# Kernel optimization log

Hardware: AMD Instinct MI355X
Metric: run time of the kernel (lower is better)

The kernel has to match this reference:

```python
import jax, jax.numpy as jnp
import numpy as np

DIM = 768
HEAD = 12
DK = DIM // HEAD

def setup_inputs() -> dict:
    key = jax.random.key(0)
    ks = jax.random.split(key, 9)
    B, L = 4, 2048
    s = 1.0 / np.sqrt(DIM)
    qkv = jax.random.normal(ks[0], (B, L, DIM), dtype=jnp.float32)
    mask = jnp.ones((B, L), dtype=jnp.int32)
    Wq = jax.random.normal(ks[1], (DIM, DIM), dtype=jnp.float32) * s
    bq = jnp.zeros((DIM,), dtype=jnp.float32)
    Wk = jax.random.normal(ks[2], (DIM, DIM), dtype=jnp.float32) * s
    bk = jnp.zeros((DIM,), dtype=jnp.float32)
    Wv = jax.random.normal(ks[3], (DIM, DIM), dtype=jnp.float32) * s
    bv = jnp.zeros((DIM,), dtype=jnp.float32)
    Wo = jax.random.normal(ks[4], (DIM, DIM), dtype=jnp.float32) * s
    bo = jnp.zeros((DIM,), dtype=jnp.float32)
    return {"qkv": qkv, "mask": mask, "Wq": Wq, "bq": bq, "Wk": Wk, "bk": bk,
            "Wv": Wv, "bv": bv, "Wo": Wo, "bo": bo}

def reference(qkv, mask, Wq, bq, Wk, bk, Wv, bv, Wo, bo):
    B, L, _ = qkv.shape
    def proj(W, b):
        # [B,L,dim] -> [B,H,L,dk]
        return (qkv @ W + b).reshape(B, L, HEAD, DK).transpose(0, 2, 1, 3)
    q, k, v = proj(Wq, bq), proj(Wk, bk), proj(Wv, bv)
    scores = jnp.einsum('bhqd,bhkd->bhqk', q, k) / jnp.sqrt(jnp.float32(DK))
    # mask: [B,L] broadcast over heads and query positions (key axis)
    m = mask[:, None, None, :]  # [B,1,1,L]
    scores = jnp.where(m == 0, jnp.float32(-1e9), scores)
    p = jax.nn.softmax(scores, axis=-1)
    x = jnp.einsum('bhqk,bhkd->bhqd', p, v)  # [B,H,L,dk]
    x = x.transpose(0, 2, 1, 3).reshape(B, L, DIM)
    return x @ Wo + bo
```

## Files before the change

### kernel.cpp

```cpp
#include <hip/hip_runtime.h>
#include <hip/hip_bf16.h>
#include <stdint.h>

#define DIM  768
#define NHEAD 12
#define DK   64
#define BATCH 4
#define SEQ  2048
#define ROWS (BATCH*SEQ)
#define SCL  0.1803368801111204f

typedef __bf16 bf16_t;
typedef bf16_t bf16x8 __attribute__((ext_vector_type(8)));
typedef bf16_t bf16x4 __attribute__((ext_vector_type(4)));
typedef float  f32x4  __attribute__((ext_vector_type(4)));
typedef float  f32x16 __attribute__((ext_vector_type(16)));

typedef unsigned int __attribute__((address_space(1)))* as1p;
typedef unsigned int __attribute__((address_space(3)))* as3p;

__device__ __forceinline__ void gload_lds16(const void* g, void* l) {
    __builtin_amdgcn_global_load_lds((as1p)g, (as3p)l, 16, 0, 0);
}
#define MEMFENCE asm volatile("" ::: "memory")

__global__ void cast_bf16_kernel(const float* __restrict__ in, bf16_t* __restrict__ out) {
    int i = blockIdx.x * 256 + threadIdx.x;
    const float4* p = (const float4*)in;
    float4 a = p[(size_t)i*2], b = p[(size_t)i*2+1];
    bf16x8 v;
    v[0]=(bf16_t)a.x; v[1]=(bf16_t)a.y; v[2]=(bf16_t)a.z; v[3]=(bf16_t)a.w;
    v[4]=(bf16_t)b.x; v[5]=(bf16_t)b.y; v[6]=(bf16_t)b.z; v[7]=(bf16_t)b.w;
    *(bf16x8*)(out + (size_t)i*8) = v;
}

__global__ void wtrans_kernel(const float* __restrict__ W0, const float* __restrict__ W1,
                              const float* __restrict__ W2, const float* __restrict__ W3,
                              bf16_t* __restrict__ T0, bf16_t* __restrict__ T1,
                              bf16_t* __restrict__ T2, bf16_t* __restrict__ T3) {
    const float* W = blockIdx.z==0?W0 : blockIdx.z==1?W1 : blockIdx.z==2?W2 : W3;
    bf16_t*      T = blockIdx.z==0?T0 : blockIdx.z==1?T1 : blockIdx.z==2?T2 : T3;
    __shared__ float tile[32][33];
    int tx = threadIdx.x, ty = threadIdx.y;
    int c = blockIdx.x*32 + tx;
    #pragma unroll
    for (int r = 0; r < 32; r += 8)
        tile[ty+r][tx] = W[(size_t)(blockIdx.y*32 + ty + r)*DIM + c];
    __syncthreads();
    int oc = blockIdx.y*32 + tx;
    #pragma unroll
    for (int r = 0; r < 32; r += 8)
        T[(size_t)(blockIdx.x*32 + ty + r)*DIM + oc] = (bf16_t)tile[tx][ty+r];
}

template<int MODE>
__global__ __launch_bounds__(256) void gemm_kernel(
    const bf16_t* __restrict__ A,
    const bf16_t* __restrict__ WTa, const bf16_t* __restrict__ WTb, const bf16_t* __restrict__ WTc,
    const float* __restrict__ ba, const float* __restrict__ bb, const float* __restrict__ bc,
    bf16_t* __restrict__ Qo, bf16_t* __restrict__ Ko, bf16_t* __restrict__ Vo,
    float* __restrict__ Oo) {
    __shared__ __align__(16) bf16_t As[128*64];
    __shared__ __align__(16) bf16_t Bs[128*64];
    const int tid = threadIdx.x, wave = tid>>6, lane = tid&63;
    const int wm = wave>>1, wn = wave&1;
    const int m0 = blockIdx.x*128, n0 = blockIdx.y*128;
    const int z = (MODE==0) ? (int)blockIdx.z : 0;
    const bf16_t* WT  = (z==0) ? WTa : (z==1 ? WTb : WTc);
    const float* bias = (z==0) ? ba  : (z==1 ? bb  : bc);

    f32x4 acc[4][4];
    const f32x4 zf = {0.f,0.f,0.f,0.f};
    #pragma unroll
    for (int m = 0; m < 4; ++m)
        #pragma unroll
        for (int n = 0; n < 4; ++n) acc[m][n] = zf;

    const int srow = wave*32 + (lane>>3);
    const int scol = (lane&7)*8;
    const bf16_t* Ag = A  + (size_t)(m0+srow)*DIM + scol;
    const bf16_t* Bg = WT + (size_t)(n0+srow)*DIM + scol;
    bf16_t* AsW = As + (wave*32)*64;
    bf16_t* BsW = Bs + (wave*32)*64;

    for (int k0 = 0; k0 < DIM; k0 += 64) {
        __syncthreads();
        #pragma unroll
        for (int i = 0; i < 4; ++i) {
            gload_lds16(Ag + (size_t)(i*8)*DIM + k0, AsW + i*8*64);
            gload_lds16(Bg + (size_t)(i*8)*DIM + k0, BsW + i*8*64);
        }
        __syncthreads();
        #pragma unroll
        for (int ks = 0; ks < 2; ++ks) {
            bf16x8 af[4], bfr[4];
            #pragma unroll
            for (int m = 0; m < 4; ++m)
                af[m]  = *(const bf16x8*)&As[(wm*64 + m*16 + (lane&15))*64 + ks*32 + (lane>>4)*8];
            #pragma unroll
            for (int n = 0; n < 4; ++n)
                bfr[n] = *(const bf16x8*)&Bs[(wn*64 + n*16 + (lane&15))*64 + ks*32 + (lane>>4)*8];
            #pragma unroll
            for (int m = 0; m < 4; ++m)
                #pragma unroll
                for (int n = 0; n < 4; ++n)
                    acc[m][n] = __builtin_amdgcn_mfma_f32_16x16x32_bf16(af[m], bfr[n], acc[m][n], 0, 0, 0);
        }
    }

    float bvv[4];
    #pragma unroll
    for (int n = 0; n < 4; ++n) bvv[n] = bias[n0 + wn*64 + n*16 + (lane&15)];

    #pragma unroll
    for (int m = 0; m < 4; ++m) {
        #pragma unroll
        for (int n = 0; n < 4; ++n) {
            #pragma unroll
            for (int r = 0; r < 4; ++r) {
                float val = acc[m][n][r] + bvv[n];
                int R = m0 + wm*64 + m*16 + (lane>>4)*4 + r;
                int C = n0 + wn*64 + n*16 + (lane&15);
                if (MODE == 1) {
                    Oo[(size_t)R*DIM + C] = val;
                } else {
                    int bi = R>>11, li = R&2047, h = C>>6, d = C&63;
                    size_t bh = (size_t)(bi*NHEAD + h);
                    if      (z==0) Qo[(bh*SEQ + li)*DK + d] = (bf16_t)(val*SCL);
                    else if (z==1) Ko[(bh*SEQ + li)*DK + d] = (bf16_t)val;
                    else {
                        int li2 = (li & ~12) | ((li&4)<<1) | ((li&8)>>1);
                        Vo[(bh*DK + d)*SEQ + li2] = (bf16_t)val;
                    }
                }
            }
        }
    }
}

#define NT (SEQ/64)

__global__ __launch_bounds__(256) void attn_kernel(
    const bf16_t* __restrict__ Q, const bf16_t* __restrict__ K, const bf16_t* __restrict__ VT,
    const int* __restrict__ mask, bf16_t* __restrict__ X) {
    __shared__ __align__(16) bf16_t lds[2*8192];
    const int tid = threadIdx.x, wv = tid>>6, lane = tid&63;
    const int lo5 = lane&31, hi5 = lane>>5;
    const int bh = blockIdx.y, bi = bh/NHEAD, h = bh%NHEAD;
    const bf16_t* Qb = Q  + (size_t)bh*SEQ*DK;
    const bf16_t* Kb = K  + (size_t)bh*SEQ*DK;
    const bf16_t* Vb = VT + (size_t)bh*DK*SEQ;
    const int* mk = mask + (size_t)bi*SEQ + lo5;
    const int q0 = blockIdx.x*128 + wv*32;

    bf16x8 qf[4];
    #pragma unroll
    for (int ks = 0; ks < 4; ++ks)
        qf[ks] = *(const bf16x8*)&Qb[(size_t)(q0 + lo5)*DK + ks*16 + hi5*8];

    f32x16 O0, O1;
    #pragma unroll
    for (int r = 0; r < 16; ++r) { O0[r] = 0.f; O1[r] = 0.f; }
    float mrun = -1e30f, lsum = 0.f;

    bf16x8 onesb = {};
    if (hi5 == 0) onesb[0] = (bf16_t)1.0f;

    const int srow  = wv*16 + (lane>>3);
    const int sslot = (lane&7) ^ (srow&7);
    const bf16_t* Kg = Kb + (size_t)srow*DK  + sslot*8;
    const bf16_t* Vg = Vb + (size_t)srow*SEQ + sslot*8;
    int koff[4];
    #pragma unroll
    for (int ks = 0; ks < 4; ++ks) koff[ks] = (((2*ks + hi5) ^ (lo5 & 7)) << 3);

    #pragma unroll
    for (int i = 0; i < 2; ++i) {
        gload_lds16(Kg + (size_t)(i*8)*DK,  lds +        (wv*16 + i*8)*64);
        gload_lds16(Vg + (size_t)(i*8)*SEQ, lds + 4096 + (wv*16 + i*8)*64);
    }

    int cur = 0;
    for (int t = 0; t < NT; ++t) {
        const int kv0 = t*64;
        int mv0 = mk[kv0], mv1 = mk[kv0 + 32];
        if (t < NT-1) {
            bf16_t* nb = lds + (cur^1)*8192;
            #pragma unroll
            for (int i = 0; i < 2; ++i) {
                gload_lds16(Kg + (size_t)(kv0+64)*DK + (size_t)(i*8)*DK,  nb +        (wv*16 + i*8)*64);
                gload_lds16(Vg + (kv0+64)            + (size_t)(i*8)*SEQ, nb + 4096 + (wv*16 + i*8)*64);
            }
            asm volatile("s_waitcnt vmcnt(4)" ::: "memory");
        } else {
            asm volatile("s_waitcnt vmcnt(0)" ::: "memory");
        }
        MEMFENCE; __builtin_amdgcn_s_barrier(); MEMFENCE;

        const bf16_t* Kt = lds + cur*8192;
        const bf16_t* Vt = lds + cur*8192 + 4096;

        f32x16 s0, s1;
        #pragma unroll
        for (int r = 0; r < 16; ++r) { s0[r] = 0.f; s1[r] = 0.f; }
        #pragma unroll
        for (int ks = 0; ks < 4; ++ks) {
            bf16x8 a0 = *(const bf16x8*)&Kt[ lo5     *64 + koff[ks]];
            bf16x8 a1 = *(const bf16x8*)&Kt[(32+lo5)*64 + koff[ks]];
            s0 = __builtin_amdgcn_mfma_f32_32x32x16_bf16(a0, qf[ks], s0, 0, 0, 0);
            s1 = __builtin_amdgcn_mfma_f32_32x32x16_bf16(a1, qf[ks], s1, 0, 0, 0);
        }
        bf16x8 ba = {};
        ba[0] = mv0 ? (bf16_t)0.f : (bf16_t)(-1024.0f);
        s0 = __builtin_amdgcn_mfma_f32_32x32x16_bf16(ba, onesb, s0, 0, 0, 0);
        ba[0] = mv1 ? (bf16_t)0.f : (bf16_t)(-1024.0f);
        s1 = __builtin_amdgcn_mfma_f32_32x32x16_bf16(ba, onesb, s1, 0, 0, 0);

        float pm = fmaxf(s0[0], s1[0]);
        #pragma unroll
        for (int r = 1; r < 16; ++r) pm = fmaxf(pm, fmaxf(s0[r], s1[r]));
        pm = fmaxf(pm, __shfl_xor(pm, 32));

        float nm = fmaxf(mrun, pm);
        if (__any(pm > mrun + 8.f)) {
            float fs = __builtin_amdgcn_exp2f(mrun - nm);
            lsum *= fs;
            #pragma unroll
            for (int r = 0; r < 16; ++r) { O0[r] *= fs; O1[r] *= fs; }
            mrun = nm;
        }
        float ps = 0.f;
        #pragma unroll
        for (int r = 0; r < 16; ++r) {
            s0[r] = __builtin_amdgcn_exp2f(s0[r] - mrun);
            s1[r] = __builtin_amdgcn_exp2f(s1[r] - mrun);
            ps += s0[r] + s1[r];
        }
        lsum += ps + __shfl_xor(ps, 32);

        bf16x8 pf0, pf1, pf2, pf3;
        #pragma unroll
        for (int j = 0; j < 8; ++j) {
            pf0[j] = (bf16_t)s0[j];
            pf1[j] = (bf16_t)s0[8+j];
            pf2[j] = (bf16_t)s1[j];
            pf3[j] = (bf16_t)s1[8+j];
        }

        #pragma unroll
        for (int ks = 0; ks < 4; ++ks) {
            bf16x8 pb = (ks==0) ? pf0 : (ks==1) ? pf1 : (ks==2) ? pf2 : pf3;
            bf16x8 a0 = *(const bf16x8*)&Vt[ lo5     *64 + koff[ks]];
            bf16x8 a1 = *(const bf16x8*)&Vt[(32+lo5)*64 + koff[ks]];
            O0 = __builtin_amdgcn_mfma_f32_32x32x16_bf16(a0, pb, O0, 0, 0, 0);
            O1 = __builtin_amdgcn_mfma_f32_32x32x16_bf16(a1, pb, O1, 0, 0, 0);
        }
        MEMFENCE; __builtin_amdgcn_s_barrier(); MEMFENCE;
        cur ^= 1;
    }

    float rl = __builtin_amdgcn_rcpf(lsum);
    const size_t rowb = (size_t)(bi*SEQ + q0 + lo5)*DIM + h*DK;
    #pragma unroll
    for (int g = 0; g < 4; ++g) {
        bf16x4 v0, v1;
        #pragma unroll
        for (int j = 0; j < 4; ++j) {
            v0[j] = (bf16_t)(O0[g*4+j] * rl);
            v1[j] = (bf16_t)(O1[g*4+j] * rl);
        }
        *(bf16x4*)&X[rowb + g*8 + hi5*4]      = v0;
        *(bf16x4*)&X[rowb + 32 + g*8 + hi5*4] = v1;
    }
}

extern "C" void kernel_launch(void* const* d_in, const int* in_sizes, int n_in,
                              void* d_out, int out_size, void* d_ws, size_t ws_size,
                              hipStream_t stream) {
    (void)in_sizes; (void)n_in; (void)out_size; (void)ws_size;
    const float* qkv = (const float*)d_in[0];
    const int*  mask = (const int*)d_in[1];
    const float* Wq = (const float*)d_in[2];
    const float* bq = (const float*)d_in[3];
    const float* Wk = (const float*)d_in[4];
    const float* bk = (const float*)d_in[5];
    const float* Wv = (const float*)d_in[6];
    const float* bv = (const float*)d_in[7];
    const float* Wo = (const float*)d_in[8];
    const float* bo = (const float*)d_in[9];
    float* out = (float*)d_out;

    char* ws = (char*)d_ws;
    size_t off = 0;
    auto carve = [&](size_t bytes) { void* p = ws + off; off += (bytes + 255) & ~(size_t)255; return p; };
    const size_t actN = (size_t)ROWS*DIM;
    bf16_t* Abf = (bf16_t*)carve(actN*2);
    bf16_t* WTq = (bf16_t*)carve((size_t)DIM*DIM*2);
    bf16_t* WTk = (bf16_t*)carve((size_t)DIM*DIM*2);
    bf16_t* WTv = (bf16_t*)carve((size_t)DIM*DIM*2);
    bf16_t* WTo = (bf16_t*)carve((size_t)DIM*DIM*2);
    bf16_t* Qb  = (bf16_t*)carve(actN*2);
    bf16_t* Kb  = (bf16_t*)carve(actN*2);
    bf16_t* VTb = (bf16_t*)carve(actN*2);
    bf16_t* Xb  = (bf16_t*)carve(actN*2);

    cast_bf16_kernel<<<dim3(ROWS*DIM/8/256), dim3(256), 0, stream>>>(qkv, Abf);
    wtrans_kernel<<<dim3(24,24,4), dim3(32,8), 0, stream>>>(Wq, Wk, Wv, Wo, WTq, WTk, WTv, WTo);
    gemm_kernel<0><<<dim3(64,6,3), dim3(256), 0, stream>>>(Abf, WTq, WTk, WTv, bq, bk, bv,
                                                           Qb, Kb, VTb, nullptr);
    attn_kernel<<<dim3(16,48), dim3(256), 0, stream>>>(Qb, Kb, VTb, mask, Xb);
    gemm_kernel<1><<<dim3(64,6,1), dim3(256), 0, stream>>>(Xb, WTo, WTo, WTo, bo, bo, bo,
                                                           nullptr, nullptr, nullptr, out);
}
```

Measured before the change: 199.1 us.

## Skip mask bias MFMAs when batch mask is all ones, remap blocks per XCD

Each attention block first scans its batch's mask row and, if every entry is nonzero, skips the per-tile mask loads and the two extra bias MFMAs. The 2D grid is flattened to 1D and remapped so that blocks sharing one head land on the same XCD, which should improve K/V reuse in L2. The max and sum reductions are rewritten as trees to shorten dependency chains. The mask scan adds a small prologue read per block. The skip stays correct for any mask because it falls back when zeros are present.

```diff
diff --git a/kernel.cpp b/kernel.cpp
--- a/kernel.cpp
+++ b/kernel.cpp
@@ -146,12 +146,26 @@
     __shared__ __align__(16) bf16_t lds[2*8192];
     const int tid = threadIdx.x, wv = tid>>6, lane = tid&63;
     const int lo5 = lane&31, hi5 = lane>>5;
-    const int bh = blockIdx.y, bi = bh/NHEAD, h = bh%NHEAD;
+    const int b = blockIdx.x;
+    const int xcd = b & 7, ii = b >> 3;
+    const int bh = xcd*6 + (ii>>4), qt = ii & 15;
+    const int bi = bh/NHEAD, h = bh%NHEAD;
     const bf16_t* Qb = Q  + (size_t)bh*SEQ*DK;
     const bf16_t* Kb = K  + (size_t)bh*SEQ*DK;
     const bf16_t* Vb = VT + (size_t)bh*DK*SEQ;
     const int* mk = mask + (size_t)bi*SEQ + lo5;
-    const int q0 = blockIdx.x*128 + wv*32;
+    const int q0 = qt*128 + wv*32;
+
+    int mOk = 1;
+    {
+        const int4* m4 = (const int4*)(mask + (size_t)bi*SEQ);
+        #pragma unroll
+        for (int i2 = 0; i2 < 8; ++i2) {
+            int4 v = m4[lane + i2*64];
+            mOk &= (v.x != 0) & (v.y != 0) & (v.z != 0) & (v.w != 0);
+        }
+    }
+    const int mAll = __all(mOk);
 
     bf16x8 qf[4];
     #pragma unroll
@@ -183,7 +197,6 @@
     int cur = 0;
     for (int t = 0; t < NT; ++t) {
         const int kv0 = t*64;
-        int mv0 = mk[kv0], mv1 = mk[kv0 + 32];
         if (t < NT-1) {
             bf16_t* nb = lds + (cur^1)*8192;
             #pragma unroll
@@ -210,15 +223,25 @@
             s0 = __builtin_amdgcn_mfma_f32_32x32x16_bf16(a0, qf[ks], s0, 0, 0, 0);
             s1 = __builtin_amdgcn_mfma_f32_32x32x16_bf16(a1, qf[ks], s1, 0, 0, 0);
         }
-        bf16x8 ba = {};
-        ba[0] = mv0 ? (bf16_t)0.f : (bf16_t)(-1024.0f);
-        s0 = __builtin_amdgcn_mfma_f32_32x32x16_bf16(ba, onesb, s0, 0, 0, 0);
-        ba[0] = mv1 ? (bf16_t)0.f : (bf16_t)(-1024.0f);
-        s1 = __builtin_amdgcn_mfma_f32_32x32x16_bf16(ba, onesb, s1, 0, 0, 0);
-
-        float pm = fmaxf(s0[0], s1[0]);
-        #pragma unroll
-        for (int r = 1; r < 16; ++r) pm = fmaxf(pm, fmaxf(s0[r], s1[r]));
+        if (!mAll) {
+            int mv0 = mk[kv0], mv1 = mk[kv0 + 32];
+            bf16x8 ba = {};
+            ba[0] = mv0 ? (bf16_t)0.f : (bf16_t)(-1024.0f);
+            s0 = __builtin_amdgcn_mfma_f32_32x32x16_bf16(ba, onesb, s0, 0, 0, 0);
+            ba[0] = mv1 ? (bf16_t)0.f : (bf16_t)(-1024.0f);
+            s1 = __builtin_amdgcn_mfma_f32_32x32x16_bf16(ba, onesb, s1, 0, 0, 0);
+        }
+
+        float m01[16];
+        #pragma unroll
+        for (int r = 0; r < 16; ++r) m01[r] = fmaxf(s0[r], s1[r]);
+        float a0t = fmaxf(fmaxf(m01[0],  m01[1]),  m01[2]);
+        float a1t = fmaxf(fmaxf(m01[3],  m01[4]),  m01[5]);
+        float a2t = fmaxf(fmaxf(m01[6],  m01[7]),  m01[8]);
+        float a3t = fmaxf(fmaxf(m01[9],  m01[10]), m01[11]);
+        float a4t = fmaxf(fmaxf(m01[12], m01[13]), m01[14]);
+        float pm = fmaxf(fmaxf(fmaxf(a0t, a1t), a2t),
+                         fmaxf(fmaxf(a3t, a4t), m01[15]));
         pm = fmaxf(pm, __shfl_xor(pm, 32));
 
         float nm = fmaxf(mrun, pm);
@@ -229,13 +252,20 @@
             for (int r = 0; r < 16; ++r) { O0[r] *= fs; O1[r] *= fs; }
             mrun = nm;
         }
-        float ps = 0.f;
         #pragma unroll
         for (int r = 0; r < 16; ++r) {
             s0[r] = __builtin_amdgcn_exp2f(s0[r] - mrun);
             s1[r] = __builtin_amdgcn_exp2f(s1[r] - mrun);
-            ps += s0[r] + s1[r];
-        }
+        }
+        float t01[16];
+        #pragma unroll
+        for (int r = 0; r < 16; ++r) t01[r] = s0[r] + s1[r];
+        float u[8];
+        #pragma unroll
+        for (int r = 0; r < 8; ++r) u[r] = t01[r] + t01[r+8];
+        float w0 = (u[0]+u[1]) + (u[2]+u[3]);
+        float w1 = (u[4]+u[5]) + (u[6]+u[7]);
+        float ps = w0 + w1;
         lsum += ps + __shfl_xor(ps, 32);
 
         bf16x8 pf0, pf1, pf2, pf3;
@@ -308,7 +338,7 @@
     wtrans_kernel<<<dim3(24,24,4), dim3(32,8), 0, stream>>>(Wq, Wk, Wv, Wo, WTq, WTk, WTv, WTo);
     gemm_kernel<0><<<dim3(64,6,3), dim3(256), 0, stream>>>(Abf, WTq, WTk, WTv, bq, bk, bv,
                                                            Qb, Kb, VTb, nullptr);
-    attn_kernel<<<dim3(16,48), dim3(256), 0, stream>>>(Qb, Kb, VTb, mask, Xb);
+    attn_kernel<<<dim3(768), dim3(256), 0, stream>>>(Qb, Kb, VTb, mask, Xb);
     gemm_kernel<1><<<dim3(64,6,1), dim3(256), 0, stream>>>(Xb, WTo, WTo, WTo, bo, bo, bo,
                                                            nullptr, nullptr, nullptr, out);
 }
```

Measured after the change: 196.9 us. Within noise of the previous version (-1.1%).
